# Kernel optimization log

Hardware: AMD Instinct MI355X
Metric: run time of the kernel (lower is better)

The kernel has to match this reference:

```python
import jax, jax.numpy as jnp
import numpy as np

B, OBS, LAT, NXT, E, HG, H = 8192, 128, 32, 128, 8, 256, 256


def setup_inputs() -> dict:
    key = jax.random.key(0)
    ks = jax.random.split(key, 20)
    d_in = OBS + LAT

    def w(k, shape, fan_in):
        return jax.random.uniform(k, shape, jnp.float32, -1.0, 1.0) * (np.sqrt(3.0) / np.sqrt(fan_in)).astype(np.float32)

    inp = {
        "x": jax.random.normal(ks[0], (B, OBS), jnp.float32),
        "z": jax.random.normal(ks[1], (B, LAT), jnp.float32),
        # gating MLP: (obs+lat) -> hg -> hg -> hg -> E
        "gw0": w(ks[2], (d_in, HG), d_in), "gb0": jnp.zeros((HG,), jnp.float32),
        "gw1": w(ks[3], (HG, HG), HG),    "gb1": jnp.zeros((HG,), jnp.float32),
        "gw2": w(ks[4], (HG, HG), HG),    "gb2": jnp.zeros((HG,), jnp.float32),
        "gw3": w(ks[5], (HG, E), HG),     "gb3": jnp.zeros((E,), jnp.float32),
        # expert weight stacks (kaiming-uniform-style init, bias = 0.01)
        "w0": w(ks[6], (E, d_in, H), d_in * H),      "b0": jnp.full((E, H), 0.01, jnp.float32),
        "w1": w(ks[7], (E, H + LAT, H), (H + LAT) * H), "b1": jnp.full((E, H), 0.01, jnp.float32),
        "w2": w(ks[8], (E, H + LAT, NXT), (H + LAT) * NXT), "b2": jnp.full((E, NXT), 0.01, jnp.float32),
    }
    return inp


def reference(x, z, gw0, gb0, gw1, gb1, gw2, gb2, gw3, gb3, w0, b0, w1, b1, w2, b2):
    xz = jnp.concatenate((x, z), axis=1)  # [B, obs+lat]
    # gating MLP (ELU activations, linear head) -> softmax coefficients over experts
    g = jax.nn.elu(xz @ gw0 + gb0)
    g = jax.nn.elu(g @ gw1 + gb1)
    g = jax.nn.elu(g @ gw2 + gb2)
    coef = jax.nn.softmax(g @ gw3 + gb3, axis=1)  # [B, E]

    layer_out = x
    for w, b, act in ((w0, b0, jax.nn.elu), (w1, b1, jax.nn.elu), (w2, b2, None)):
        inp = jnp.concatenate((layer_out, z), axis=1)  # [B, i]
        # coefficient-weighted expert mixing fused with the per-sample matvec:
        # equals (coef @ flat_weight).view(B,i,o) consumed by baddbmm in the original
        out = jnp.einsum('bi,eio,be->bo', inp, w, coef) + coef @ b
        layer_out = act(out) if act is not None else out
    return layer_out
```

## Files before the change

### kernel.cpp

```cpp
#include <hip/hip_runtime.h>
#include <hip/hip_bf16.h>

typedef _Float16 half_t;
typedef __attribute__((ext_vector_type(8))) _Float16 half8;
typedef __attribute__((ext_vector_type(4))) _Float16 half4;
typedef __attribute__((ext_vector_type(4))) float float4v;

#define BSZ 8192
#define NT 1024

#define RING_SLOT 1024
#define RING_WAVE (3 * RING_SLOT)
#define OFF_SX   (16 * RING_WAVE)
#define OFF_SB0  (OFF_SX + 32 * 136)
#define OFF_SB1  (OFF_SB0 + 32 * 264)
#define OFF_SZ   (OFF_SB1 + 32 * 264)
#define HALFS_TOTAL (OFF_SZ + 32 * 40)
#define OFF_BIAS_B (HALFS_TOTAL * 2)
#define OFF_LOG_B  (OFF_BIAS_B + 8192)
#define OFF_CF_B   (OFF_LOG_B + 1024)
#define SMEM_BYTES (OFF_CF_B + 1024)

__device__ __forceinline__ float elu_fast(float v) {
    return v > 0.f ? v : (__expf(v) - 1.f);
}

template <int N>
__device__ __forceinline__ void wait_vm() {
    if constexpr (N == 0)      asm volatile("s_waitcnt vmcnt(0)" ::: "memory");
    else if constexpr (N == 1) asm volatile("s_waitcnt vmcnt(1)" ::: "memory");
    else if constexpr (N == 2) asm volatile("s_waitcnt vmcnt(2)" ::: "memory");
    else                       asm volatile("s_waitcnt vmcnt(4)" ::: "memory");
}

__device__ __forceinline__ void lds_dma16(half_t* lds, const half_t* g) {
    __builtin_amdgcn_global_load_lds(
        (const __attribute__((address_space(1))) void*)g,
        (__attribute__((address_space(3))) void*)lds, 16, 0, 0);
}

template <int EXPP, int NPASS, int CH, int MT, bool ZLAST, int ACT, int DST>
__device__ __forceinline__ void layer_run(
    half_t* sm, const half_t* sSrc, int sstr,
    const half_t* __restrict__ W, int Npad,
    const float* __restrict__ bias, int biasN, const float* sCf, float* sBias,
    half_t* sDst, float* __restrict__ gOut, int ldg,
    int row0, int strip, int mrow, int wv, int lane, int l15, int quad) {
    constexpr int K = CH * 32;
    constexpr int TOT = NPASS * CH;
    const size_t estr = (size_t)Npad * K;
    const int col = strip * 16 + l15;
    half_t* ring = sm + wv * RING_WAVE;
    const half_t* sZ = sm + OFF_SZ;
    float* myBias = sBias + wv * 128;

    if (quad == 0) {
#pragma unroll
        for (int e = 0; e < NPASS * EXPP; ++e)
            myBias[e * 16 + l15] = bias[e * biasN + col];
    }
    wait_vm<0>();

    float4v acc[EXPP][MT];
    float part[MT][4];

    const half_t* wp = &W[(size_t)col * K + quad * 8];
    int s_i = 0, c_i = 0;
    auto issue = [&]() {
        half_t* slot = ring + s_i * RING_SLOT;
#pragma unroll
        for (int e = 0; e < EXPP; ++e) lds_dma16(slot + e * 512, wp + (size_t)e * estr);
        s_i = (s_i == 2) ? 0 : s_i + 1;
        wp += 32;
        if (++c_i == CH) { c_i = 0; wp += (size_t)EXPP * estr - K; }
    };

    int s_c = 0, c_c = 0, h_c = 0;
    auto body = [&]() {
        half8 a[MT];
#pragma unroll
        for (int mt = 0; mt < MT; ++mt) {
            const int row = mrow + mt * 16 + l15;
            a[mt] = (ZLAST && c_c == CH - 1)
                        ? *(const half8*)&sZ[row * 40 + quad * 8]
                        : *(const half8*)&sSrc[row * sstr + c_c * 32 + quad * 8];
        }
        if (c_c == 0) {
#pragma unroll
            for (int e = 0; e < EXPP; ++e)
#pragma unroll
                for (int mt = 0; mt < MT; ++mt) acc[e][mt] = (float4v){0.f, 0.f, 0.f, 0.f};
        }
        const half_t* slot = ring + s_c * RING_SLOT + lane * 8;
#pragma unroll
        for (int e = 0; e < EXPP; ++e) {
            half8 b = *(const half8*)&slot[e * 512];
#pragma unroll
            for (int mt = 0; mt < MT; ++mt)
                acc[e][mt] = __builtin_amdgcn_mfma_f32_16x16x32_f16(a[mt], b, acc[e][mt], 0, 0, 0);
        }
        if (c_c == CH - 1) {
            const int eoff = h_c * EXPP;
#pragma unroll
            for (int mt = 0; mt < MT; ++mt)
#pragma unroll
                for (int r = 0; r < 4; ++r) {
                    const int rl = mrow + mt * 16 + quad * 4 + r;
                    float val = 0.f;
#pragma unroll
                    for (int e = 0; e < EXPP; ++e) {
                        const float ab = acc[e][mt][r] + myBias[(eoff + e) * 16 + l15];
                        val += (EXPP * NPASS == 1) ? ab : sCf[rl * 8 + eoff + e] * ab;
                    }
                    part[mt][r] = (h_c == 0) ? val : part[mt][r] + val;
                    if (h_c == NPASS - 1) {
                        float o = part[mt][r];
                        if (DST == 0) {
                            if (ACT) o = elu_fast(o);
                            sDst[rl * 264 + col] = (half_t)o;
                        } else {
                            gOut[(size_t)(row0 + rl) * ldg + col] = o;
                        }
                    }
                }
        }
        s_c = (s_c == 2) ? 0 : s_c + 1;
        if (++c_c == CH) { c_c = 0; ++h_c; }
    };

    issue();
    issue();
#pragma unroll 1
    for (int it = 0; it < TOT - 2; ++it) {
        issue();
        wait_vm<2 * EXPP>();
        body();
    }
    wait_vm<EXPP>();
    body();
    wait_vm<0>();
    body();
}

__device__ __forceinline__ void layer_logits(
    const half_t* sSrc, const half_t* __restrict__ W,
    const float* __restrict__ bias, float* sLog, int wv, int l15, int quad) {
    if (wv != 0) return;
    float4v acc[2] = {(float4v){0.f, 0.f, 0.f, 0.f}, (float4v){0.f, 0.f, 0.f, 0.f}};
    const half_t* wb = &W[(size_t)l15 * 256 + quad * 8];
#pragma unroll
    for (int c = 0; c < 8; ++c) {
        half8 a0 = *(const half8*)&sSrc[l15 * 264 + c * 32 + quad * 8];
        half8 a1 = *(const half8*)&sSrc[(16 + l15) * 264 + c * 32 + quad * 8];
        half8 b = *(const half8*)&wb[c * 32];
        acc[0] = __builtin_amdgcn_mfma_f32_16x16x32_f16(a0, b, acc[0], 0, 0, 0);
        acc[1] = __builtin_amdgcn_mfma_f32_16x16x32_f16(a1, b, acc[1], 0, 0, 0);
    }
    if (l15 < 8) {
        const float bvv = bias[l15];
#pragma unroll
        for (int mt = 0; mt < 2; ++mt)
#pragma unroll
            for (int r = 0; r < 4; ++r)
                sLog[(mt * 16 + quad * 4 + r) * 8 + l15] = acc[mt][r] + bvv;
    }
}

__global__ __launch_bounds__(NT) void fused_mann(
    const float* __restrict__ x, const float* __restrict__ z,
    const half_t* __restrict__ Wg0, const half_t* __restrict__ Wg1,
    const half_t* __restrict__ Wg2, const half_t* __restrict__ Wg3,
    const float* __restrict__ gb0, const float* __restrict__ gb1,
    const float* __restrict__ gb2, const float* __restrict__ gb3,
    const half_t* __restrict__ W0, const half_t* __restrict__ W1,
    const half_t* __restrict__ W2, const float* __restrict__ b0,
    const float* __restrict__ b1, const float* __restrict__ b2,
    float* __restrict__ out) {
    extern __shared__ __align__(16) char dynsm[];
    half_t* sm = (half_t*)dynsm;
    half_t* sX = sm + OFF_SX;
    half_t* sB0 = sm + OFF_SB0;
    half_t* sB1 = sm + OFF_SB1;
    half_t* sZ = sm + OFF_SZ;
    float* sBias = (float*)(dynsm + OFF_BIAS_B);
    float* sLog = (float*)(dynsm + OFF_LOG_B);
    float* sCf = (float*)(dynsm + OFF_CF_B);

    const int tid = threadIdx.x;
    const int row0 = blockIdx.x * 32;
    const int lane = tid & 63, wv = tid >> 6;
    const int l15 = lane & 15, quad = lane >> 4;

    for (int i = tid; i < 32 * 128; i += NT) {
        int r = i >> 7, c = i & 127;
        sX[r * 136 + c] = (half_t)x[(size_t)(row0 + r) * 128 + c];
    }
    for (int i = tid; i < 32 * 32; i += NT) {
        int r = i >> 5, c = i & 31;
        sZ[r * 40 + c] = (half_t)z[(size_t)(row0 + r) * 32 + c];
    }
    __syncthreads();

    layer_run<1, 1, 5, 2, true, 1, 0>(sm, sX, 136, Wg0, 256, gb0, 256, nullptr, sBias,
                                      sB0, nullptr, 0, row0, wv, 0, wv, lane, l15, quad);
    __syncthreads();
    layer_run<1, 1, 8, 2, false, 1, 0>(sm, sB0, 264, Wg1, 256, gb1, 256, nullptr, sBias,
                                       sB1, nullptr, 0, row0, wv, 0, wv, lane, l15, quad);
    __syncthreads();
    layer_run<1, 1, 8, 2, false, 1, 0>(sm, sB1, 264, Wg2, 256, gb2, 256, nullptr, sBias,
                                       sB0, nullptr, 0, row0, wv, 0, wv, lane, l15, quad);
    __syncthreads();
    layer_logits(sB0, Wg3, gb3, sLog, wv, l15, quad);
    __syncthreads();
    if (tid < 32) {
        float v[8], m = -1e30f;
#pragma unroll
        for (int e = 0; e < 8; ++e) { v[e] = sLog[tid * 8 + e]; m = fmaxf(m, v[e]); }
        float sum = 0.f;
#pragma unroll
        for (int e = 0; e < 8; ++e) { v[e] = __expf(v[e] - m); sum += v[e]; }
        float inv = 1.f / sum;
#pragma unroll
        for (int e = 0; e < 8; ++e) sCf[tid * 8 + e] = v[e] * inv;
    }
    __syncthreads();
    layer_run<2, 4, 5, 2, true, 1, 0>(sm, sX, 136, W0, 256, b0, 256, sCf, sBias,
                                      sB1, nullptr, 0, row0, wv, 0, wv, lane, l15, quad);
    __syncthreads();
    layer_run<2, 4, 9, 2, true, 1, 0>(sm, sB1, 264, W1, 256, b1, 256, sCf, sBias,
                                      sB0, nullptr, 0, row0, wv, 0, wv, lane, l15, quad);
    __syncthreads();
    layer_run<2, 4, 9, 1, true, 0, 2>(sm, sB0, 264, W2, 128, b2, 128, sCf, sBias,
                                      nullptr, out, 128, row0, wv & 7, (wv >> 3) * 16,
                                      wv, lane, l15, quad);
}

struct WDesc { const float* src; half_t* dst; int K, N, Npad, blk0; };
struct WPack { WDesc d[7]; };

__global__ __launch_bounds__(256) void conv_w_all(WPack pk) {
    __shared__ float t[32][33];
    const int bid = blockIdx.x;
    int di = 0;
#pragma unroll
    for (int i = 1; i < 7; ++i)
        if (bid >= pk.d[i].blk0) di = i;
    const WDesc d = pk.d[di];
    const int ntiles = d.Npad / 32, ktiles = d.K / 32;
    int local = bid - d.blk0;
    const int e = local / (ktiles * ntiles);
    local %= ktiles * ntiles;
    const int k0 = (local / ntiles) * 32, n0 = (local % ntiles) * 32;
    const int tr = threadIdx.x >> 3;
    const int tc = (threadIdx.x & 7) * 4;

    float4 v = {0.f, 0.f, 0.f, 0.f};
    if (n0 + tc < d.N)
        v = *(const float4*)&d.src[((size_t)e * d.K + k0 + tr) * d.N + n0 + tc];
    t[tr][tc] = v.x; t[tr][tc + 1] = v.y; t[tr][tc + 2] = v.z; t[tr][tc + 3] = v.w;
    __syncthreads();
    half4 h;
#pragma unroll
    for (int i = 0; i < 4; ++i) h[i] = (half_t)t[tc + i][tr];
    *(half4*)&d.dst[((size_t)e * d.Npad + n0 + tr) * d.K + k0 + tc] = h;
}

extern "C" void kernel_launch(void* const* d_in, const int* in_sizes, int n_in,
                              void* d_out, int out_size, void* d_ws, size_t ws_size,
                              hipStream_t stream) {
    const float* x   = (const float*)d_in[0];
    const float* z   = (const float*)d_in[1];
    const float* gw0 = (const float*)d_in[2];
    const float* gb0 = (const float*)d_in[3];
    const float* gw1 = (const float*)d_in[4];
    const float* gb1 = (const float*)d_in[5];
    const float* gw2 = (const float*)d_in[6];
    const float* gb2 = (const float*)d_in[7];
    const float* gw3 = (const float*)d_in[8];
    const float* gb3 = (const float*)d_in[9];
    const float* w0  = (const float*)d_in[10];
    const float* b0  = (const float*)d_in[11];
    const float* w1  = (const float*)d_in[12];
    const float* b1  = (const float*)d_in[13];
    const float* w2  = (const float*)d_in[14];
    const float* b2  = (const float*)d_in[15];

    char* p = (char*)d_ws;
    auto take = [&](size_t bytes) { char* r = p; p += bytes; return r; };
    half_t* Wg0 = (half_t*)take((size_t)256 * 160 * 2);
    half_t* Wg1 = (half_t*)take((size_t)256 * 256 * 2);
    half_t* Wg2 = (half_t*)take((size_t)256 * 256 * 2);
    half_t* Wg3 = (half_t*)take((size_t)32 * 256 * 2);
    half_t* W0  = (half_t*)take((size_t)8 * 256 * 160 * 2);
    half_t* W1  = (half_t*)take((size_t)8 * 256 * 288 * 2);
    half_t* W2  = (half_t*)take((size_t)8 * 128 * 288 * 2);
    float* out  = (float*)d_out;

    WPack pk;
    int blk = 0;
    auto mk = [&](int i, const float* s, half_t* dst, int K, int N, int Npad, int E) {
        pk.d[i] = WDesc{s, dst, K, N, Npad, blk};
        blk += E * (K / 32) * (Npad / 32);
    };
    mk(0, gw0, Wg0, 160, 256, 256, 1);
    mk(1, gw1, Wg1, 256, 256, 256, 1);
    mk(2, gw2, Wg2, 256, 256, 256, 1);
    mk(3, gw3, Wg3, 256, 8, 32, 1);
    mk(4, w0, W0, 160, 256, 256, 8);
    mk(5, w1, W1, 288, 256, 256, 8);
    mk(6, w2, W2, 288, 128, 128, 8);

    hipFuncSetAttribute((const void*)fused_mann,
                        hipFuncAttributeMaxDynamicSharedMemorySize, SMEM_BYTES);

    conv_w_all<<<dim3(blk), dim3(256), 0, stream>>>(pk);
    fused_mann<<<dim3(BSZ / 32), dim3(NT), SMEM_BYTES, stream>>>(
        x, z, Wg0, Wg1, Wg2, Wg3, gb0, gb1, gb2, gb3,
        W0, W1, W2, b0, b1, b2, out);
}
```

Measured before the change: 158.1 us.

## Pre-tile weights into MFMA fragment blocks and pad LDS activation strides

The weight conversion kernel now writes each 16-column by 32-K chunk as one contiguous 512-half block in MFMA B-fragment order. The global-to-LDS DMA in the main kernel therefore reads fully contiguous 1 KB per wave per chunk instead of 16 strided rows. LDS row strides for the activation, x and z buffers change (264→280, 136→152) to alter the bank mapping of the A-operand reads, and row base pointers are hoisted out of the inner loop. The layout change has to stay consistent between the conversion kernel and every consumer, including the logits head.

```diff
diff --git a/kernel.cpp b/kernel.cpp
--- a/kernel.cpp
+++ b/kernel.cpp
@@ -8,14 +8,17 @@
 
 #define BSZ 8192
 #define NT 1024
+#define ACTSTR 280
+#define XSTR 152
+#define ZSTR 40
 
 #define RING_SLOT 1024
 #define RING_WAVE (3 * RING_SLOT)
 #define OFF_SX   (16 * RING_WAVE)
-#define OFF_SB0  (OFF_SX + 32 * 136)
-#define OFF_SB1  (OFF_SB0 + 32 * 264)
-#define OFF_SZ   (OFF_SB1 + 32 * 264)
-#define HALFS_TOTAL (OFF_SZ + 32 * 40)
+#define OFF_SB0  (OFF_SX + 32 * XSTR)
+#define OFF_SB1  (OFF_SB0 + 32 * ACTSTR)
+#define OFF_SZ   (OFF_SB1 + 32 * ACTSTR)
+#define HALFS_TOTAL (OFF_SZ + 32 * ZSTR)
 #define OFF_BIAS_B (HALFS_TOTAL * 2)
 #define OFF_LOG_B  (OFF_BIAS_B + 8192)
 #define OFF_CF_B   (OFF_LOG_B + 1024)
@@ -42,13 +45,12 @@
 template <int EXPP, int NPASS, int CH, int MT, bool ZLAST, int ACT, int DST>
 __device__ __forceinline__ void layer_run(
     half_t* sm, const half_t* sSrc, int sstr,
-    const half_t* __restrict__ W, int Npad,
+    const half_t* __restrict__ W, int NS,
     const float* __restrict__ bias, int biasN, const float* sCf, float* sBias,
     half_t* sDst, float* __restrict__ gOut, int ldg,
     int row0, int strip, int mrow, int wv, int lane, int l15, int quad) {
-    constexpr int K = CH * 32;
     constexpr int TOT = NPASS * CH;
-    const size_t estr = (size_t)Npad * K;
+    const size_t estr = (size_t)NS * CH * 512;
     const int col = strip * 16 + l15;
     half_t* ring = sm + wv * RING_WAVE;
     const half_t* sZ = sm + OFF_SZ;
@@ -64,27 +66,27 @@
     float4v acc[EXPP][MT];
     float part[MT][4];
 
-    const half_t* wp = &W[(size_t)col * K + quad * 8];
+    const half_t* wp = W + (size_t)strip * CH * 512 + lane * 8;
     int s_i = 0, c_i = 0;
     auto issue = [&]() {
         half_t* slot = ring + s_i * RING_SLOT;
 #pragma unroll
         for (int e = 0; e < EXPP; ++e) lds_dma16(slot + e * 512, wp + (size_t)e * estr);
         s_i = (s_i == 2) ? 0 : s_i + 1;
-        wp += 32;
-        if (++c_i == CH) { c_i = 0; wp += (size_t)EXPP * estr - K; }
+        wp += 512;
+        if (++c_i == CH) { c_i = 0; wp += EXPP * estr - CH * 512; }
     };
 
+    const half_t* aBase = sSrc + (mrow + l15) * sstr + quad * 8;
+    const half_t* zBase = sZ + (mrow + l15) * ZSTR + quad * 8;
     int s_c = 0, c_c = 0, h_c = 0;
     auto body = [&]() {
         half8 a[MT];
 #pragma unroll
-        for (int mt = 0; mt < MT; ++mt) {
-            const int row = mrow + mt * 16 + l15;
+        for (int mt = 0; mt < MT; ++mt)
             a[mt] = (ZLAST && c_c == CH - 1)
-                        ? *(const half8*)&sZ[row * 40 + quad * 8]
-                        : *(const half8*)&sSrc[row * sstr + c_c * 32 + quad * 8];
-        }
+                        ? *(const half8*)&zBase[mt * 16 * ZSTR]
+                        : *(const half8*)&aBase[mt * 16 * sstr + c_c * 32];
         if (c_c == 0) {
 #pragma unroll
             for (int e = 0; e < EXPP; ++e)
@@ -117,7 +119,7 @@
                         float o = part[mt][r];
                         if (DST == 0) {
                             if (ACT) o = elu_fast(o);
-                            sDst[rl * 264 + col] = (half_t)o;
+                            sDst[rl * ACTSTR + col] = (half_t)o;
                         } else {
                             gOut[(size_t)(row0 + rl) * ldg + col] = o;
                         }
@@ -144,15 +146,14 @@
 
 __device__ __forceinline__ void layer_logits(
     const half_t* sSrc, const half_t* __restrict__ W,
-    const float* __restrict__ bias, float* sLog, int wv, int l15, int quad) {
+    const float* __restrict__ bias, float* sLog, int wv, int lane, int l15, int quad) {
     if (wv != 0) return;
     float4v acc[2] = {(float4v){0.f, 0.f, 0.f, 0.f}, (float4v){0.f, 0.f, 0.f, 0.f}};
-    const half_t* wb = &W[(size_t)l15 * 256 + quad * 8];
 #pragma unroll
     for (int c = 0; c < 8; ++c) {
-        half8 a0 = *(const half8*)&sSrc[l15 * 264 + c * 32 + quad * 8];
-        half8 a1 = *(const half8*)&sSrc[(16 + l15) * 264 + c * 32 + quad * 8];
-        half8 b = *(const half8*)&wb[c * 32];
+        half8 a0 = *(const half8*)&sSrc[l15 * ACTSTR + c * 32 + quad * 8];
+        half8 a1 = *(const half8*)&sSrc[(16 + l15) * ACTSTR + c * 32 + quad * 8];
+        half8 b = *(const half8*)&W[c * 512 + lane * 8];
         acc[0] = __builtin_amdgcn_mfma_f32_16x16x32_f16(a0, b, acc[0], 0, 0, 0);
         acc[1] = __builtin_amdgcn_mfma_f32_16x16x32_f16(a1, b, acc[1], 0, 0, 0);
     }
@@ -193,24 +194,24 @@
 
     for (int i = tid; i < 32 * 128; i += NT) {
         int r = i >> 7, c = i & 127;
-        sX[r * 136 + c] = (half_t)x[(size_t)(row0 + r) * 128 + c];
+        sX[r * XSTR + c] = (half_t)x[(size_t)(row0 + r) * 128 + c];
     }
     for (int i = tid; i < 32 * 32; i += NT) {
         int r = i >> 5, c = i & 31;
-        sZ[r * 40 + c] = (half_t)z[(size_t)(row0 + r) * 32 + c];
-    }
-    __syncthreads();
-
-    layer_run<1, 1, 5, 2, true, 1, 0>(sm, sX, 136, Wg0, 256, gb0, 256, nullptr, sBias,
+        sZ[r * ZSTR + c] = (half_t)z[(size_t)(row0 + r) * 32 + c];
+    }
+    __syncthreads();
+
+    layer_run<1, 1, 5, 2, true, 1, 0>(sm, sX, XSTR, Wg0, 16, gb0, 256, nullptr, sBias,
                                       sB0, nullptr, 0, row0, wv, 0, wv, lane, l15, quad);
     __syncthreads();
-    layer_run<1, 1, 8, 2, false, 1, 0>(sm, sB0, 264, Wg1, 256, gb1, 256, nullptr, sBias,
+    layer_run<1, 1, 8, 2, false, 1, 0>(sm, sB0, ACTSTR, Wg1, 16, gb1, 256, nullptr, sBias,
                                        sB1, nullptr, 0, row0, wv, 0, wv, lane, l15, quad);
     __syncthreads();
-    layer_run<1, 1, 8, 2, false, 1, 0>(sm, sB1, 264, Wg2, 256, gb2, 256, nullptr, sBias,
+    layer_run<1, 1, 8, 2, false, 1, 0>(sm, sB1, ACTSTR, Wg2, 16, gb2, 256, nullptr, sBias,
                                        sB0, nullptr, 0, row0, wv, 0, wv, lane, l15, quad);
     __syncthreads();
-    layer_logits(sB0, Wg3, gb3, sLog, wv, l15, quad);
+    layer_logits(sB0, Wg3, gb3, sLog, wv, lane, l15, quad);
     __syncthreads();
     if (tid < 32) {
         float v[8], m = -1e30f;
@@ -224,13 +225,13 @@
         for (int e = 0; e < 8; ++e) sCf[tid * 8 + e] = v[e] * inv;
     }
     __syncthreads();
-    layer_run<2, 4, 5, 2, true, 1, 0>(sm, sX, 136, W0, 256, b0, 256, sCf, sBias,
+    layer_run<2, 4, 5, 2, true, 1, 0>(sm, sX, XSTR, W0, 16, b0, 256, sCf, sBias,
                                       sB1, nullptr, 0, row0, wv, 0, wv, lane, l15, quad);
     __syncthreads();
-    layer_run<2, 4, 9, 2, true, 1, 0>(sm, sB1, 264, W1, 256, b1, 256, sCf, sBias,
+    layer_run<2, 4, 9, 2, true, 1, 0>(sm, sB1, ACTSTR, W1, 16, b1, 256, sCf, sBias,
                                       sB0, nullptr, 0, row0, wv, 0, wv, lane, l15, quad);
     __syncthreads();
-    layer_run<2, 4, 9, 1, true, 0, 2>(sm, sB0, 264, W2, 128, b2, 128, sCf, sBias,
+    layer_run<2, 4, 9, 1, true, 0, 2>(sm, sB0, ACTSTR, W2, 8, b2, 128, sCf, sBias,
                                       nullptr, out, 128, row0, wv & 7, (wv >> 3) * 16,
                                       wv, lane, l15, quad);
 }
@@ -246,7 +247,8 @@
     for (int i = 1; i < 7; ++i)
         if (bid >= pk.d[i].blk0) di = i;
     const WDesc d = pk.d[di];
-    const int ntiles = d.Npad / 32, ktiles = d.K / 32;
+    const int NS = d.Npad >> 4, CHN = d.K >> 5;
+    const int ntiles = d.Npad / 32, ktiles = CHN;
     int local = bid - d.blk0;
     const int e = local / (ktiles * ntiles);
     local %= ktiles * ntiles;
@@ -262,7 +264,10 @@
     half4 h;
 #pragma unroll
     for (int i = 0; i < 4; ++i) h[i] = (half_t)t[tc + i][tr];
-    *(half4*)&d.dst[((size_t)e * d.Npad + n0 + tr) * d.K + k0 + tc] = h;
+    const int n = n0 + tr;
+    const size_t blk = ((size_t)e * NS + (n >> 4)) * CHN + (k0 >> 5);
+    const int off = ((tc >> 3) * 16 + (n & 15)) * 8 + (tc & 7);
+    *(half4*)&d.dst[blk * 512 + off] = h;
 }
 
 extern "C" void kernel_launch(void* const* d_in, const int* in_sizes, int n_in,
```

Result: faster. 137.9 us, median of 2 (-12.8%).
